# Kernel tuning notes

Measured on AMD Instinct MI355X. Metric: run time of the kernel, lower is better.

Reference implementation:

```python
import jax, jax.numpy as jnp
import numpy as np

N = 100000    # nodes
E = 800000    # directed edges
EF = 16       # edge features
NF = 1        # node features (forced by the module's MLP-size constraint)
HID = NF * 8  # NNConv out = 8
H1, C1 = 8, 16  # gat1 heads / per-head channels -> 128
NC = 16       # num_classes (gat2: heads=1, out=NC)


def setup_inputs() -> dict:
    key = jax.random.key(0)
    ks = jax.random.split(key, 20)
    s = 0.1
    return {
        "x": jax.random.normal(ks[0], (N, NF), jnp.float32),
        "edge_index": jax.random.randint(ks[1], (2, E), 0, N, jnp.int64),
        "edge_attr": jax.random.normal(ks[2], (E, EF), jnp.float32),
        # edge MLP: Linear(EF,8) -> ReLU -> Linear(8,8)
        "w1": jax.random.normal(ks[3], (EF, HID), jnp.float32) * s,
        "b1": jnp.zeros((HID,), jnp.float32),
        "w2": jax.random.normal(ks[4], (HID, HID), jnp.float32) * s,
        "b2": jnp.zeros((HID,), jnp.float32),
        # NNConv root weight + bias
        "root": jax.random.normal(ks[5], (NF, HID), jnp.float32) * s,
        "nn_bias": jnp.zeros((HID,), jnp.float32),
        # GAT1: in 8 -> 16 ch x 8 heads
        "g1W": jax.random.normal(ks[6], (HID, H1 * C1), jnp.float32) * s,
        "g1as": jax.random.normal(ks[7], (H1, C1), jnp.float32) * s,
        "g1ad": jax.random.normal(ks[8], (H1, C1), jnp.float32) * s,
        "g1b": jnp.zeros((H1 * C1,), jnp.float32),
        # GAT2: in 128 -> NC, 1 head
        "g2W": jax.random.normal(ks[9], (H1 * C1, NC), jnp.float32) * s,
        "g2as": jax.random.normal(ks[10], (1, NC), jnp.float32) * s,
        "g2ad": jax.random.normal(ks[11], (1, NC), jnp.float32) * s,
        "g2b": jnp.zeros((NC,), jnp.float32),
    }


def _gat(h_in, W, a_src, a_dst, bias, src, dst, n, heads, ch):
    # h: [N, heads, ch]
    h = (h_in @ W).reshape(n, heads, ch)
    e_s = jnp.einsum("nhc,hc->nh", h, a_src)   # per-node src logits
    e_d = jnp.einsum("nhc,hc->nh", h, a_dst)
    e = jax.nn.leaky_relu(e_s[src] + e_d[dst], 0.2)      # [E2, heads]
    m = jax.ops.segment_max(e, dst, num_segments=n)      # segment softmax
    e = jnp.exp(e - m[dst])
    z = jax.ops.segment_sum(e, dst, num_segments=n)
    alpha = e / (z[dst] + 1e-16)                          # [E2, heads]
    out = jax.ops.segment_sum(alpha[:, :, None] * h[src], dst, num_segments=n)
    return out.reshape(n, heads * ch) + bias


def reference(x, edge_index, edge_attr, w1, b1, w2, b2, root, nn_bias,
              g1W, g1as, g1ad, g1b, g2W, g2as, g2ad, g2b):
    n = x.shape[0]
    src, dst = edge_index[0], edge_index[1]

    # ---- NNConv (aggr='mean'): per-edge weight from edge MLP ----
    w_e = jax.nn.relu(edge_attr @ w1 + b1) @ w2 + b2      # [E, NF*HID]
    w_e = w_e.reshape(-1, NF, HID)
    msg = jnp.einsum("ei,eio->eo", x[src], w_e)            # [E, HID]
    sums = jax.ops.segment_sum(msg, dst, num_segments=n)
    cnt = jax.ops.segment_sum(jnp.ones((msg.shape[0],), msg.dtype), dst, num_segments=n)
    aggr = sums / jnp.maximum(cnt, 1.0)[:, None]
    h = jax.nn.relu(aggr + x @ root + nn_bias)             # [N, 8]
    # dropout: eval mode -> identity

    # ---- add self-loops (PyG GATConv default) ----
    loops = jnp.arange(n, dtype=src.dtype)
    src2 = jnp.concatenate([src, loops])
    dst2 = jnp.concatenate([dst, loops])

    h = jax.nn.elu(_gat(h, g1W, g1as, g1ad, g1b, src2, dst2, n, H1, C1))  # [N,128]
    out = _gat(h, g2W, g2as, g2ad, g2b, src2, dst2, n, 1, NC)             # [N,16]
    return jax.nn.log_softmax(out, axis=1)
```

## Files before the change

kernel.cpp:

```cpp
#include <hip/hip_runtime.h>
#include <hip/hip_fp16.h>
#include <math.h>

constexpr int NN  = 100000;
constexpr int NE  = 800000;
constexpr int H1 = 8, C1 = 16;
constexpr int D1 = H1 * C1;
constexpr int NC = 16;
constexpr int SCAN_B = 256;
constexpr int SCAN_NB = (NN + SCAN_B - 1) / SCAN_B;

static inline int cdiv(int a, int b) { return (a + b - 1) / b; }

__device__ inline __half2 h2_bits(unsigned u) {
    __half2 r; __builtin_memcpy(&r, &u, 4); return r;
}
__device__ inline __half2 shflx_h2(__half2 v, int off) {
    int iv; __builtin_memcpy(&iv, &v, 4);
    iv = __shfl_xor(iv, off);
    __half2 r; __builtin_memcpy(&r, &iv, 4); return r;
}

__global__ void hist_kernel(const int* __restrict__ dst, int* __restrict__ deg) {
    int e = blockIdx.x * blockDim.x + threadIdx.x;
    if (e < NE) atomicAdd(&deg[dst[e]], 1);
}

__global__ void scan1(const int* __restrict__ deg, int* __restrict__ row,
                      int* __restrict__ partial) {
    __shared__ int s[SCAN_B];
    int tid = threadIdx.x;
    int i = blockIdx.x * SCAN_B + tid;
    int v = (i < NN) ? deg[i] : 0;
    s[tid] = v;
    __syncthreads();
    for (int off = 1; off < SCAN_B; off <<= 1) {
        int t = 0;
        if (tid >= off) t = s[tid - off];
        __syncthreads();
        s[tid] += t;
        __syncthreads();
    }
    if (i < NN) row[i] = s[tid] - v;
    if (tid == SCAN_B - 1) partial[blockIdx.x] = s[tid];
}

__global__ void scan2(int* __restrict__ partial, int nb) {
    __shared__ int s[512];
    int tid = threadIdx.x;
    int v = (tid < nb) ? partial[tid] : 0;
    s[tid] = v;
    __syncthreads();
    for (int off = 1; off < 512; off <<= 1) {
        int t = 0;
        if (tid >= off) t = s[tid - off];
        __syncthreads();
        s[tid] += t;
        __syncthreads();
    }
    if (tid < nb) partial[tid] = s[tid] - v;
}

__global__ void scan3(int* __restrict__ row, const int* __restrict__ partial,
                      int* __restrict__ cursor) {
    int i = blockIdx.x * SCAN_B + threadIdx.x;
    if (i < NN) {
        int r = row[i] + partial[blockIdx.x];
        row[i] = r;
        cursor[i] = r;
    }
}

__global__ void nnconv_scatter(const float* __restrict__ x,
                               const int* __restrict__ src, const int* __restrict__ dst,
                               const float* __restrict__ ea,
                               const float* __restrict__ w1, const float* __restrict__ b1,
                               const float* __restrict__ w2, const float* __restrict__ b2,
                               int* __restrict__ cursor,
                               int* __restrict__ src_s, __half* __restrict__ msg_s) {
    __shared__ float sw1[16 * 8], sw2[8 * 8], sb1[8], sb2[8];
    int t = threadIdx.x;
    if (t < 128) sw1[t] = w1[t];
    else if (t < 192) sw2[t - 128] = w2[t - 128];
    else if (t < 200) sb1[t - 192] = b1[t - 192];
    else if (t < 208) sb2[t - 200] = b2[t - 200];
    __syncthreads();
    int e = blockIdx.x * blockDim.x + t;
    if (e >= NE) return;

    float a[16];
    const float4* ea4 = (const float4*)(ea + (size_t)e * 16);
    float4 v0 = ea4[0], v1 = ea4[1], v2 = ea4[2], v3 = ea4[3];
    a[0]=v0.x; a[1]=v0.y; a[2]=v0.z; a[3]=v0.w;
    a[4]=v1.x; a[5]=v1.y; a[6]=v1.z; a[7]=v1.w;
    a[8]=v2.x; a[9]=v2.y; a[10]=v2.z; a[11]=v2.w;
    a[12]=v3.x; a[13]=v3.y; a[14]=v3.z; a[15]=v3.w;

    float hdn[8];
#pragma unroll
    for (int j = 0; j < 8; j++) {
        float s = sb1[j];
#pragma unroll
        for (int i = 0; i < 16; i++) s = fmaf(a[i], sw1[i * 8 + j], s);
        hdn[j] = fmaxf(s, 0.f);
    }
    int sn = src[e], dn = dst[e];
    float xv = x[sn];
    __align__(16) __half msg[8];
#pragma unroll
    for (int j = 0; j < 8; j++) {
        float s = sb2[j];
#pragma unroll
        for (int i = 0; i < 8; i++) s = fmaf(hdn[i], sw2[i * 8 + j], s);
        msg[j] = __float2half(xv * s);
    }
    int pos = atomicAdd(&cursor[dn], 1);
    src_s[pos] = sn;
    *(uint4*)(msg_s + (size_t)pos * 8) = *(const uint4*)msg;
}

__global__ void fused_node1(const float* __restrict__ x,
                            const int* __restrict__ row, const int* __restrict__ deg,
                            const __half* __restrict__ msg_s,
                            const float* __restrict__ root, const float* __restrict__ nb,
                            const float* __restrict__ W,
                            const float* __restrict__ as_, const float* __restrict__ ad_,
                            __half* __restrict__ h1h,
                            float* __restrict__ es, float* __restrict__ ed) {
    int t = blockIdx.x * blockDim.x + threadIdx.x;
    if (t >= NN * 8) return;
    int n = t >> 3, j = t & 7;
    int rs = row[n], d = deg[n];
    float sum = 0.f;
    for (int p = rs; p < rs + d; p++) sum += __half2float(msg_s[(size_t)p * 8 + j]);
    float hj = fmaxf(sum / fmaxf((float)d, 1.f) + x[n] * root[j] + nb[j], 0.f);

    float hv[8];
#pragma unroll
    for (int k = 0; k < 8; k++) hv[k] = __shfl(hj, k, 8);

    int hd = j;
    float acc[16];
#pragma unroll
    for (int c = 0; c < 16; c++) acc[c] = 0.f;
#pragma unroll
    for (int k = 0; k < 8; k++) {
        const float* wr = W + k * D1 + hd * 16;
#pragma unroll
        for (int c = 0; c < 16; c++) acc[c] = fmaf(hv[k], wr[c], acc[c]);
    }
    float s = 0.f, dd = 0.f;
    __align__(16) __half hh[16];
#pragma unroll
    for (int c = 0; c < 16; c++) {
        s = fmaf(acc[c], as_[hd * 16 + c], s);
        dd = fmaf(acc[c], ad_[hd * 16 + c], dd);
        hh[c] = __float2half(acc[c]);
    }
    float4* hp = (float4*)(h1h + (size_t)n * D1 + hd * 16);
    hp[0] = ((const float4*)hh)[0];
    hp[1] = ((const float4*)hh)[1];
    es[t] = s;
    ed[t] = dd;
}

__global__ __launch_bounds__(256) void gat1_gather(
        const int* __restrict__ row, const int* __restrict__ deg,
        const int* __restrict__ src_s,
        const float* __restrict__ es, const float* __restrict__ ed,
        const __half* __restrict__ h1h, const float* __restrict__ b,
        const float* __restrict__ W2,
        const float* __restrict__ as2, const float* __restrict__ ad2,
        __half* __restrict__ h2h, float* __restrict__ es2, float* __restrict__ ed2) {
    __shared__ float sW2[2048];
    __shared__ float so[4][4][132];
    int tid = threadIdx.x;
    for (int idx = tid; idx < 2048; idx += 256) sW2[idx] = W2[idx];
    __syncthreads();

    int wv = tid >> 6, lane = tid & 63;
    int g  = lane >> 4;
    int cl = lane & 15;
    int hd = cl >> 1;
    const uint4* h1h4 = (const uint4*)h1h;
    float4 bv0 = *((const float4*)(b + cl * 8));
    float4 bv1 = *((const float4*)(b + cl * 8 + 4));

    int base = (blockIdx.x * 4 + wv) * 4;
    for (int i = 0; i < 4; i++) {
        int node = base + i;
        int rs = row[node], d = deg[node];
        float edn = ed[node * 8 + hd];

        float vs = es[node * 8 + hd] + edn;
        vs = fmaxf(vs, 0.2f * vs);
        float a0 = (g == 0) ? __expf(vs) : 0.f;
        float z = a0;
        __half2 ap = __float2half2_rn(a0);
        uint4 gl = h1h4[(unsigned)node * 16u + (unsigned)cl];
        __half2 acc0 = __hmul2(ap, h2_bits(gl.x));
        __half2 acc1 = __hmul2(ap, h2_bits(gl.y));
        __half2 acc2 = __hmul2(ap, h2_bits(gl.z));
        __half2 acc3 = __hmul2(ap, h2_bits(gl.w));

        for (int k = g; k < d; k += 4) {
            int s = src_s[rs + k];
            float v = es[(unsigned)s * 8u + hd] + edn;
            v = fmaxf(v, 0.2f * v);
            float a = __expf(v);
            uint4 ge = h1h4[(unsigned)s * 16u + (unsigned)cl];
            __half2 a2 = __float2half2_rn(a);
            z += a;
            acc0 = __hfma2(a2, h2_bits(ge.x), acc0);
            acc1 = __hfma2(a2, h2_bits(ge.y), acc1);
            acc2 = __hfma2(a2, h2_bits(ge.z), acc2);
            acc3 = __hfma2(a2, h2_bits(ge.w), acc3);
        }
        z += __shfl_xor(z, 16); z += __shfl_xor(z, 32);
        acc0 = __hadd2(acc0, shflx_h2(acc0, 16)); acc0 = __hadd2(acc0, shflx_h2(acc0, 32));
        acc1 = __hadd2(acc1, shflx_h2(acc1, 16)); acc1 = __hadd2(acc1, shflx_h2(acc1, 32));
        acc2 = __hadd2(acc2, shflx_h2(acc2, 16)); acc2 = __hadd2(acc2, shflx_h2(acc2, 32));
        acc3 = __hadd2(acc3, shflx_h2(acc3, 16)); acc3 = __hadd2(acc3, shflx_h2(acc3, 32));

        float rz = 1.f / (z + 1e-16f);
        float2 f0 = __half22float2(acc0), f1 = __half22float2(acc1);
        float2 f2 = __half22float2(acc2), f3 = __half22float2(acc3);
        float o0 = fmaf(f0.x, rz, bv0.x), o1 = fmaf(f0.y, rz, bv0.y);
        float o2 = fmaf(f1.x, rz, bv0.z), o3 = fmaf(f1.y, rz, bv0.w);
        float o4 = fmaf(f2.x, rz, bv1.x), o5 = fmaf(f2.y, rz, bv1.y);
        float o6 = fmaf(f3.x, rz, bv1.z), o7 = fmaf(f3.y, rz, bv1.w);
        o0 = o0 > 0.f ? o0 : expm1f(o0);
        o1 = o1 > 0.f ? o1 : expm1f(o1);
        o2 = o2 > 0.f ? o2 : expm1f(o2);
        o3 = o3 > 0.f ? o3 : expm1f(o3);
        o4 = o4 > 0.f ? o4 : expm1f(o4);
        o5 = o5 > 0.f ? o5 : expm1f(o5);
        o6 = o6 > 0.f ? o6 : expm1f(o6);
        o7 = o7 > 0.f ? o7 : expm1f(o7);
        if (g == 0) {
            float4* sp = (float4*)&so[wv][i][cl * 8];
            sp[0] = make_float4(o0, o1, o2, o3);
            sp[1] = make_float4(o4, o5, o6, o7);
        }
    }
    __asm__ __volatile__("s_waitcnt lgkmcnt(0)" ::: "memory");

    int nl = lane >> 4, c = lane & 15;
    float partial = 0.f;
#pragma unroll 4
    for (int k = 0; k < 128; k += 2) {
        float2 sv = *(const float2*)&so[wv][nl][k];
        partial = fmaf(sv.x, sW2[k * 16 + c], partial);
        partial = fmaf(sv.y, sW2[(k + 1) * 16 + c], partial);
    }
    float ta = partial * as2[c], tb = partial * ad2[c];
#pragma unroll
    for (int off = 1; off < 16; off <<= 1) {
        ta += __shfl_xor(ta, off);
        tb += __shfl_xor(tb, off);
    }
    h2h[(size_t)(base + nl) * 16 + c] = __float2half(partial);
    if (c == 0) { es2[base + nl] = ta; ed2[base + nl] = tb; }
}

__global__ __launch_bounds__(256) void gat2_gather(
        const int* __restrict__ row, const int* __restrict__ deg,
        const int* __restrict__ src_s,
        const float* __restrict__ es, const float* __restrict__ ed,
        const __half* __restrict__ h2h, const float* __restrict__ b,
        float* __restrict__ out) {
    int tid = threadIdx.x;
    int wv = tid >> 6, lane = tid & 63;
    int g = lane >> 3, l = lane & 7;
    const __half2* h2h2 = (const __half2*)h2h;
    float2 bv = ((const float2*)b)[l];
    int base = (blockIdx.x * 4 + wv) * 4;
    for (int i = 0; i < 4; i++) {
        int node = base + i;
        int rs = row[node], d = deg[node];
        float edn = ed[node];
        float vs = es[node] + edn;
        vs = fmaxf(vs, 0.2f * vs);
        float a0 = (g == 0) ? __expf(vs) : 0.f;
        float z = a0;
        __half2 acc = __hmul2(__float2half2_rn(a0), h2h2[(unsigned)node * 8u + l]);

        for (int k = g; k < d; k += 8) {
            int s = src_s[rs + k];
            float v = es[s] + edn;
            v = fmaxf(v, 0.2f * v);
            float a = __expf(v);
            __half2 hv = h2h2[(unsigned)s * 8u + l];
            z += a;
            acc = __hfma2(__float2half2_rn(a), hv, acc);
        }
        z += __shfl_xor(z, 8); z += __shfl_xor(z, 16); z += __shfl_xor(z, 32);
        acc = __hadd2(acc, shflx_h2(acc, 8));
        acc = __hadd2(acc, shflx_h2(acc, 16));
        acc = __hadd2(acc, shflx_h2(acc, 32));

        float rz = 1.f / (z + 1e-16f);
        float2 f = __half22float2(acc);
        float o0 = fmaf(f.x, rz, bv.x);
        float o1 = fmaf(f.y, rz, bv.y);
        float mx = fmaxf(o0, o1);
        mx = fmaxf(mx, __shfl_xor(mx, 1));
        mx = fmaxf(mx, __shfl_xor(mx, 2));
        mx = fmaxf(mx, __shfl_xor(mx, 4));
        float ss = __expf(o0 - mx) + __expf(o1 - mx);
        ss += __shfl_xor(ss, 1); ss += __shfl_xor(ss, 2); ss += __shfl_xor(ss, 4);
        float lg = mx + __logf(ss);
        if (g == 0)
            ((float2*)out)[(unsigned)node * 8u + l] = make_float2(o0 - lg, o1 - lg);
    }
}

extern "C" void kernel_launch(void* const* d_in, const int* in_sizes, int n_in,
                              void* d_out, int out_size, void* d_ws, size_t ws_size,
                              hipStream_t stream) {
    const float* x    = (const float*)d_in[0];
    const int*   ei   = (const int*)d_in[1];
    const float* ea   = (const float*)d_in[2];
    const float* w1   = (const float*)d_in[3];
    const float* b1   = (const float*)d_in[4];
    const float* w2   = (const float*)d_in[5];
    const float* b2   = (const float*)d_in[6];
    const float* root = (const float*)d_in[7];
    const float* nb   = (const float*)d_in[8];
    const float* g1W  = (const float*)d_in[9];
    const float* g1as = (const float*)d_in[10];
    const float* g1ad = (const float*)d_in[11];
    const float* g1b  = (const float*)d_in[12];
    const float* g2W  = (const float*)d_in[13];
    const float* g2as = (const float*)d_in[14];
    const float* g2ad = (const float*)d_in[15];
    const float* g2b  = (const float*)d_in[16];
    float* out = (float*)d_out;

    const int* src = ei;
    const int* dst = ei + NE;

    float* ws = (float*)d_ws;
    size_t o = 0;
    __half* msg_s  = (__half*)(ws + o); o += (size_t)NE * 4;
    __half* h1h    = (__half*)(ws + o); o += (size_t)NN * D1 / 2;
    __half* h2h    = (__half*)(ws + o); o += (size_t)NN * NC / 2;
    int*  src_s = (int*)(ws + o); o += NE;
    int*  deg   = (int*)(ws + o); o += NN;
    int*  row   = (int*)(ws + o); o += NN;
    int*  cur   = (int*)(ws + o); o += NN;
    int*  part  = (int*)(ws + o); o += 512;
    float* es1  = ws + o; o += (size_t)NN * H1;
    float* ed1  = ws + o; o += (size_t)NN * H1;
    float* es2  = ws + o; o += NN;
    float* ed2  = ws + o; o += NN;
    (void)ws_size; (void)in_sizes; (void)n_in; (void)out_size;

    const int B = 256;

    hipMemsetAsync(deg, 0, (size_t)NN * sizeof(int), stream);
    hist_kernel<<<cdiv(NE, B), B, 0, stream>>>(dst, deg);
    scan1<<<SCAN_NB, SCAN_B, 0, stream>>>(deg, row, part);
    scan2<<<1, 512, 0, stream>>>(part, SCAN_NB);
    scan3<<<SCAN_NB, SCAN_B, 0, stream>>>(row, part, cur);

    nnconv_scatter<<<cdiv(NE, B), B, 0, stream>>>(x, src, dst, ea, w1, b1, w2, b2,
                                                  cur, src_s, msg_s);
    fused_node1<<<cdiv(NN * 8, B), B, 0, stream>>>(x, row, deg, msg_s, root, nb,
                                                   g1W, g1as, g1ad, h1h, es1, ed1);
    gat1_gather<<<NN / 16, B, 0, stream>>>(row, deg, src_s, es1, ed1, h1h,
                                           g1b, g2W, g2as, g2ad, h2h, es2, ed2);
    gat2_gather<<<NN / 16, B, 0, stream>>>(row, deg, src_s, es2, ed2, h2h, g2b, out);
}
```

Baseline: 352.8 us.

## Store messages in edge order with (src,edge) pairs, add nontemporal loads/stores, fast ELU

```diff
diff --git a/kernel.cpp b/kernel.cpp
--- a/kernel.cpp
+++ b/kernel.cpp
@@ -12,7 +12,10 @@
 
 static inline int cdiv(int a, int b) { return (a + b - 1) / b; }
 
-__device__ inline __half2 h2_bits(unsigned u) {
+typedef int   v4i __attribute__((ext_vector_type(4)));
+typedef int   v2i __attribute__((ext_vector_type(2)));
+
+__device__ inline __half2 h2_bits(int u) {
     __half2 r; __builtin_memcpy(&r, &u, 4); return r;
 }
 __device__ inline __half2 shflx_h2(__half2 v, int off) {
@@ -77,7 +80,7 @@
                                const float* __restrict__ w1, const float* __restrict__ b1,
                                const float* __restrict__ w2, const float* __restrict__ b2,
                                int* __restrict__ cursor,
-                               int* __restrict__ src_s, __half* __restrict__ msg_s) {
+                               int* __restrict__ pe, __half* __restrict__ msg_s) {
     __shared__ float sw1[16 * 8], sw2[8 * 8], sb1[8], sb2[8];
     int t = threadIdx.x;
     if (t < 128) sw1[t] = w1[t];
@@ -114,13 +117,16 @@
         for (int i = 0; i < 8; i++) s = fmaf(hdn[i], sw2[i * 8 + j], s);
         msg[j] = __float2half(xv * s);
     }
+    v4i mv; __builtin_memcpy(&mv, msg, 16);
+    __builtin_nontemporal_store(mv, (v4i*)(msg_s + (size_t)e * 8));
     int pos = atomicAdd(&cursor[dn], 1);
-    src_s[pos] = sn;
-    *(uint4*)(msg_s + (size_t)pos * 8) = *(const uint4*)msg;
+    v2i pv; pv[0] = sn; pv[1] = e;
+    __builtin_nontemporal_store(pv, (v2i*)(pe + (size_t)pos * 2));
 }
 
 __global__ void fused_node1(const float* __restrict__ x,
                             const int* __restrict__ row, const int* __restrict__ deg,
+                            const int* __restrict__ pe,
                             const __half* __restrict__ msg_s,
                             const float* __restrict__ root, const float* __restrict__ nb,
                             const float* __restrict__ W,
@@ -132,7 +138,10 @@
     int n = t >> 3, j = t & 7;
     int rs = row[n], d = deg[n];
     float sum = 0.f;
-    for (int p = rs; p < rs + d; p++) sum += __half2float(msg_s[(size_t)p * 8 + j]);
+    for (int p = rs; p < rs + d; p++) {
+        int eid = pe[(size_t)p * 2 + 1];
+        sum += __half2float(msg_s[(size_t)eid * 8 + j]);
+    }
     float hj = fmaxf(sum / fmaxf((float)d, 1.f) + x[n] * root[j] + nb[j], 0.f);
 
     float hv[8];
@@ -157,16 +166,19 @@
         dd = fmaf(acc[c], ad_[hd * 16 + c], dd);
         hh[c] = __float2half(acc[c]);
     }
-    float4* hp = (float4*)(h1h + (size_t)n * D1 + hd * 16);
-    hp[0] = ((const float4*)hh)[0];
-    hp[1] = ((const float4*)hh)[1];
-    es[t] = s;
+    v4i hv0, hv1;
+    __builtin_memcpy(&hv0, &hh[0], 16);
+    __builtin_memcpy(&hv1, &hh[8], 16);
+    __half* hp = h1h + (size_t)n * D1 + hd * 16;
+    __builtin_nontemporal_store(hv0, (v4i*)hp);
+    __builtin_nontemporal_store(hv1, (v4i*)(hp + 8));
+    __builtin_nontemporal_store(s, es + t);
     ed[t] = dd;
 }
 
 __global__ __launch_bounds__(256) void gat1_gather(
         const int* __restrict__ row, const int* __restrict__ deg,
-        const int* __restrict__ src_s,
+        const int* __restrict__ pe,
         const float* __restrict__ es, const float* __restrict__ ed,
         const __half* __restrict__ h1h, const float* __restrict__ b,
         const float* __restrict__ W2,
@@ -182,7 +194,6 @@
     int g  = lane >> 4;
     int cl = lane & 15;
     int hd = cl >> 1;
-    const uint4* h1h4 = (const uint4*)h1h;
     float4 bv0 = *((const float4*)(b + cl * 8));
     float4 bv1 = *((const float4*)(b + cl * 8 + 4));
 
@@ -197,24 +208,26 @@
         float a0 = (g == 0) ? __expf(vs) : 0.f;
         float z = a0;
         __half2 ap = __float2half2_rn(a0);
-        uint4 gl = h1h4[(unsigned)node * 16u + (unsigned)cl];
-        __half2 acc0 = __hmul2(ap, h2_bits(gl.x));
-        __half2 acc1 = __hmul2(ap, h2_bits(gl.y));
-        __half2 acc2 = __hmul2(ap, h2_bits(gl.z));
-        __half2 acc3 = __hmul2(ap, h2_bits(gl.w));
+        v4i gl = __builtin_nontemporal_load(
+            (const v4i*)(h1h + (size_t)node * D1 + cl * 8));
+        __half2 acc0 = __hmul2(ap, h2_bits(gl[0]));
+        __half2 acc1 = __hmul2(ap, h2_bits(gl[1]));
+        __half2 acc2 = __hmul2(ap, h2_bits(gl[2]));
+        __half2 acc3 = __hmul2(ap, h2_bits(gl[3]));
 
         for (int k = g; k < d; k += 4) {
-            int s = src_s[rs + k];
+            int s = pe[(size_t)(rs + k) * 2];
             float v = es[(unsigned)s * 8u + hd] + edn;
             v = fmaxf(v, 0.2f * v);
             float a = __expf(v);
-            uint4 ge = h1h4[(unsigned)s * 16u + (unsigned)cl];
+            v4i ge = __builtin_nontemporal_load(
+                (const v4i*)(h1h + (size_t)s * D1 + cl * 8));
             __half2 a2 = __float2half2_rn(a);
             z += a;
-            acc0 = __hfma2(a2, h2_bits(ge.x), acc0);
-            acc1 = __hfma2(a2, h2_bits(ge.y), acc1);
-            acc2 = __hfma2(a2, h2_bits(ge.z), acc2);
-            acc3 = __hfma2(a2, h2_bits(ge.w), acc3);
+            acc0 = __hfma2(a2, h2_bits(ge[0]), acc0);
+            acc1 = __hfma2(a2, h2_bits(ge[1]), acc1);
+            acc2 = __hfma2(a2, h2_bits(ge[2]), acc2);
+            acc3 = __hfma2(a2, h2_bits(ge[3]), acc3);
         }
         z += __shfl_xor(z, 16); z += __shfl_xor(z, 32);
         acc0 = __hadd2(acc0, shflx_h2(acc0, 16)); acc0 = __hadd2(acc0, shflx_h2(acc0, 32));
@@ -229,14 +242,14 @@
         float o2 = fmaf(f1.x, rz, bv0.z), o3 = fmaf(f1.y, rz, bv0.w);
         float o4 = fmaf(f2.x, rz, bv1.x), o5 = fmaf(f2.y, rz, bv1.y);
         float o6 = fmaf(f3.x, rz, bv1.z), o7 = fmaf(f3.y, rz, bv1.w);
-        o0 = o0 > 0.f ? o0 : expm1f(o0);
-        o1 = o1 > 0.f ? o1 : expm1f(o1);
-        o2 = o2 > 0.f ? o2 : expm1f(o2);
-        o3 = o3 > 0.f ? o3 : expm1f(o3);
-        o4 = o4 > 0.f ? o4 : expm1f(o4);
-        o5 = o5 > 0.f ? o5 : expm1f(o5);
-        o6 = o6 > 0.f ? o6 : expm1f(o6);
-        o7 = o7 > 0.f ? o7 : expm1f(o7);
+        o0 = o0 > 0.f ? o0 : __expf(o0) - 1.f;
+        o1 = o1 > 0.f ? o1 : __expf(o1) - 1.f;
+        o2 = o2 > 0.f ? o2 : __expf(o2) - 1.f;
+        o3 = o3 > 0.f ? o3 : __expf(o3) - 1.f;
+        o4 = o4 > 0.f ? o4 : __expf(o4) - 1.f;
+        o5 = o5 > 0.f ? o5 : __expf(o5) - 1.f;
+        o6 = o6 > 0.f ? o6 : __expf(o6) - 1.f;
+        o7 = o7 > 0.f ? o7 : __expf(o7) - 1.f;
         if (g == 0) {
             float4* sp = (float4*)&so[wv][i][cl * 8];
             sp[0] = make_float4(o0, o1, o2, o3);
@@ -259,20 +272,25 @@
         ta += __shfl_xor(ta, off);
         tb += __shfl_xor(tb, off);
     }
-    h2h[(size_t)(base + nl) * 16 + c] = __float2half(partial);
-    if (c == 0) { es2[base + nl] = ta; ed2[base + nl] = tb; }
+    __half ph = __float2half(partial);
+    short praw; __builtin_memcpy(&praw, &ph, 2);
+    __builtin_nontemporal_store(praw, (short*)(h2h + (size_t)(base + nl) * 16 + c));
+    if (c == 0) {
+        __builtin_nontemporal_store(ta, es2 + base + nl);
+        ed2[base + nl] = tb;
+    }
 }
 
 __global__ __launch_bounds__(256) void gat2_gather(
         const int* __restrict__ row, const int* __restrict__ deg,
-        const int* __restrict__ src_s,
+        const int* __restrict__ pe,
         const float* __restrict__ es, const float* __restrict__ ed,
         const __half* __restrict__ h2h, const float* __restrict__ b,
         float* __restrict__ out) {
     int tid = threadIdx.x;
     int wv = tid >> 6, lane = tid & 63;
     int g = lane >> 3, l = lane & 7;
-    const __half2* h2h2 = (const __half2*)h2h;
+    const int* h2i = (const int*)h2h;
     float2 bv = ((const float2*)b)[l];
     int base = (blockIdx.x * 4 + wv) * 4;
     for (int i = 0; i < 4; i++) {
@@ -283,16 +301,17 @@
         vs = fmaxf(vs, 0.2f * vs);
         float a0 = (g == 0) ? __expf(vs) : 0.f;
         float z = a0;
-        __half2 acc = __hmul2(__float2half2_rn(a0), h2h2[(unsigned)node * 8u + l]);
+        __half2 acc = __hmul2(__float2half2_rn(a0),
+                              h2_bits(h2i[(unsigned)node * 8u + l]));
 
         for (int k = g; k < d; k += 8) {
-            int s = src_s[rs + k];
+            int s = pe[(size_t)(rs + k) * 2];
             float v = es[s] + edn;
             v = fmaxf(v, 0.2f * v);
             float a = __expf(v);
-            __half2 hv = h2h2[(unsigned)s * 8u + l];
+            int hraw = __builtin_nontemporal_load(h2i + (unsigned)s * 8u + l);
             z += a;
-            acc = __hfma2(__float2half2_rn(a), hv, acc);
+            acc = __hfma2(__float2half2_rn(a), h2_bits(hraw), acc);
         }
         z += __shfl_xor(z, 8); z += __shfl_xor(z, 16); z += __shfl_xor(z, 32);
         acc = __hadd2(acc, shflx_h2(acc, 8));
@@ -345,7 +364,7 @@
     __half* msg_s  = (__half*)(ws + o); o += (size_t)NE * 4;
     __half* h1h    = (__half*)(ws + o); o += (size_t)NN * D1 / 2;
     __half* h2h    = (__half*)(ws + o); o += (size_t)NN * NC / 2;
-    int*  src_s = (int*)(ws + o); o += NE;
+    int*  pe    = (int*)(ws + o); o += (size_t)NE * 2;
     int*  deg   = (int*)(ws + o); o += NN;
     int*  row   = (int*)(ws + o); o += NN;
     int*  cur   = (int*)(ws + o); o += NN;
@@ -365,10 +384,10 @@
     scan3<<<SCAN_NB, SCAN_B, 0, stream>>>(row, part, cur);
 
     nnconv_scatter<<<cdiv(NE, B), B, 0, stream>>>(x, src, dst, ea, w1, b1, w2, b2,
-                                                  cur, src_s, msg_s);
-    fused_node1<<<cdiv(NN * 8, B), B, 0, stream>>>(x, row, deg, msg_s, root, nb,
+                                                  cur, pe, msg_s);
+    fused_node1<<<cdiv(NN * 8, B), B, 0, stream>>>(x, row, deg, pe, msg_s, root, nb,
                                                    g1W, g1as, g1ad, h1h, es1, ed1);
-    gat1_gather<<<NN / 16, B, 0, stream>>>(row, deg, src_s, es1, ed1, h1h,
+    gat1_gather<<<NN / 16, B, 0, stream>>>(row, deg, pe, es1, ed1, h1h,
                                            g1b, g2W, g2as, g2ad, h2h, es2, ed2);
-    gat2_gather<<<NN / 16, B, 0, stream>>>(row, deg, src_s, es2, ed2, h2h, g2b, out);
-}
+    gat2_gather<<<NN / 16, B, 0, stream>>>(row, deg, pe, es2, ed2, h2h, g2b, out);
+}
```

Result: slower. 377.7 us (+7.0%).
